# Kernel optimization log

Measured on AMD Instinct MI355X. Metric: run time of the kernel, lower is better.

## Reference

```python
import jax, jax.numpy as jnp
import numpy as np
from jax import lax


def squash(s):
    # scale = |s|^2/(1+|s|^2); out = scale * s/|s| (eps-stabilized as in source)
    norm = jnp.sum(s * s, axis=-1, keepdims=True)
    return (norm / (1.0 + norm)) * (s / jnp.sqrt(norm + 1e-8))


def setup_inputs() -> dict:
    key = jax.random.key(0)
    k = jax.random.split(key, 4)
    B, H, C = 32, 64, 10
    x = jax.random.normal(k[0], (B, 3, H, H), jnp.float32)
    conv1_w = jax.random.normal(k[1], (256, 3, 9, 9), jnp.float32) * 0.06
    conv1_b = jnp.zeros((256,), jnp.float32)
    conv2_w = jax.random.normal(k[2], (256, 256, 9, 9), jnp.float32) * 0.02  # 256 = 8 caps * 32 routes
    conv2_b = jnp.zeros((256,), jnp.float32)
    route_w = jax.random.normal(k[3], (32, C, 8, 16), jnp.float32)  # [routes, classes, in_dim, out_dim]
    return {"x": x, "conv1_w": conv1_w, "conv1_b": conv1_b,
            "conv2_w": conv2_w, "conv2_b": conv2_b, "route_w": route_w}


def reference(x, conv1_w, conv1_b, conv2_w, conv2_b, route_w):
    dn = ("NCHW", "OIHW", "NCHW")
    # PrimaryCapsules: conv 3->256 k9 s1 + relu
    h = lax.conv_general_dilated(x, conv1_w, (1, 1), "VALID", dimension_numbers=dn)
    h = jax.nn.relu(h + conv1_b[None, :, None, None])
    # CapsuleLayer conv: 256 -> 8*32 k9 s2
    h = lax.conv_general_dilated(h, conv2_w, (2, 2), "VALID", dimension_numbers=dn)
    h = h + conv2_b[None, :, None, None]
    B, _, hh, ww = h.shape
    R, D = 32, 8  # num_routes, capsule dim
    # [B, R*D, h, w] -> [B, R, P, D], squash per capsule vector
    caps = h.reshape(B, R, D, hh, ww).transpose(0, 1, 3, 4, 2).reshape(B, R, hh * ww, D)
    caps = squash(caps)
    # DigitCapsules: per-route linear maps 8->16, shared over spatial positions
    u_hat = jnp.einsum("brpi,rcio->brpco", caps, route_w)  # [B, R, P, C, 16]
    C, O = u_hat.shape[3], u_hat.shape[4]
    u_hat = u_hat.reshape(B, R * hh * ww, C, O)  # [B, N, C, 16]
    b_log = jnp.zeros(u_hat.shape[:-1], u_hat.dtype)  # [B, N, C]
    num_routing = 3
    v = None
    for i in range(num_routing):
        c = jax.nn.softmax(b_log, axis=2)            # over classes (dim=2 in source)
        s = jnp.einsum("bnc,bnco->bco", c, u_hat)    # weighted sum over input caps
        v = squash(s)                                 # [B, C, 16]
        if i < num_routing - 1:
            b_log = b_log + jnp.einsum("bnco,bco->bnc", u_hat, v)  # agreement
    return v
```

## Files before the change

kernel.cpp:

```cpp
#include <hip/hip_runtime.h>
#include <hip/hip_bf16.h>
#include <stdint.h>

typedef __attribute__((ext_vector_type(8))) short short8;
typedef __attribute__((ext_vector_type(4))) float f32x4;
typedef unsigned int u32x4a __attribute__((vector_size(16)));
typedef unsigned int u32x4u __attribute__((vector_size(16), aligned(4)));

__device__ inline unsigned short f2bf(float f) {
    union { float f; uint32_t u; } v; v.f = f;
    uint32_t u = v.u;
    uint32_t r = (u + 0x7FFFu + ((u >> 16) & 1u)) >> 16;
    return (unsigned short)r;
}

__device__ inline void gl_lds16(const unsigned short* g, unsigned short* l) {
    __builtin_amdgcn_global_load_lds(
        (const uint32_t __attribute__((address_space(1)))*)(const void*)g,
        (uint32_t __attribute__((address_space(3)))*)(void*)l, 16, 0, 0);
}

__global__ void cvt_w1(const float* __restrict__ w, unsigned short* __restrict__ A1) {
    int idx = blockIdx.x * 256 + threadIdx.x;
    int row = idx >> 8, k = idx & 255;
    float v = (k < 243) ? w[row * 243 + k] : 0.f;
    A1[idx] = f2bf(v);
}

__global__ void cvt_w2(const float* __restrict__ w, unsigned short* __restrict__ A2t) {
    int idx = blockIdx.x * 256 + threadIdx.x;
    int j = idx & 7;
    int off16 = (idx >> 3) & 1023;
    int tile = idx >> 13;
    int tm = tile / 324, chunk = tile - tm * 324;
    int row = off16 >> 3, sw = off16 & 7;
    int koct = sw ^ (row & 7);
    int kk = chunk * 64 + koct * 8 + j;
    int oc = tm * 128 + row;
    int ic, ky, kx;
    if (kk < 18432) { ic = kk / 72; int rem = kk - ic * 72; ky = rem >> 3; kx = rem & 7; }
    else { int j2 = kk - 18432; ic = j2 / 9; ky = j2 - ic * 9; kx = 8; }
    A2t[idx] = f2bf(w[((oc * 256 + ic) * 9 + ky) * 9 + kx]);
}

__global__ __launch_bounds__(256) void conv1_gemm(
    const unsigned short* __restrict__ A,
    const float* __restrict__ x,
    const float* __restrict__ bias,
    unsigned short* __restrict__ h1)
{
    __shared__ __align__(16) unsigned short As[128 * 40];
    __shared__ __align__(16) unsigned short Bs[128 * 40];
    const int tid = threadIdx.x;
    const int m0 = blockIdx.y * 128;
    const int n0 = blockIdx.x * 128;
    const int lane = tid & 63;
    const int wave = tid >> 6;
    const int wy = wave & 1, wx = wave >> 1;
    const int l16 = lane & 15, q = lane >> 4;

    const int kp = tid & 15;
    const int gn = tid >> 4;
    int baseN[8];
#pragma unroll
    for (int j = 0; j < 8; ++j) {
        int n = n0 + gn * 8 + j;
        int b = n / 3136, p = n % 3136;
        int oy = p / 56, ox = p % 56;
        baseN[j] = b * 12288 + oy * 64 + ox;
    }

    f32x4 acc[4][4];
#pragma unroll
    for (int im = 0; im < 4; ++im)
#pragma unroll
        for (int in = 0; in < 4; ++in)
            acc[im][in] = (f32x4){0.f, 0.f, 0.f, 0.f};

    for (int k0 = 0; k0 < 256; k0 += 32) {
        __syncthreads();
#pragma unroll
        for (int s = 0; s < 2; ++s) {
            int slot = tid + s * 256;
            int row = slot >> 2, seg = slot & 3;
            u32x4a v = *(const u32x4a*)(A + (m0 + row) * 256 + k0 + seg * 8);
            *(u32x4a*)(&As[row * 40 + seg * 8]) = v;
        }
        int ka = k0 + 2 * kp, kb = ka + 1;
        int offa = 0, offb = 0;
        bool va = ka < 243, vb = kb < 243;
        if (va) { int c = ka / 81, t = ka % 81, ky = t / 9, kx = t % 9; offa = c * 4096 + ky * 64 + kx; }
        if (vb) { int c = kb / 81, t = kb % 81, ky = t / 9, kx = t % 9; offb = c * 4096 + ky * 64 + kx; }
#pragma unroll
        for (int j = 0; j < 8; ++j) {
            unsigned int ba = va ? (unsigned int)f2bf(x[baseN[j] + offa]) : 0u;
            unsigned int bb = vb ? (unsigned int)f2bf(x[baseN[j] + offb]) : 0u;
            *(unsigned int*)(&Bs[(gn * 8 + j) * 40 + 2 * kp]) = ba | (bb << 16);
        }
        __syncthreads();

        short8 af[4], bf[4];
#pragma unroll
        for (int im = 0; im < 4; ++im)
            af[im] = *(const short8*)(&As[(wy * 64 + im * 16 + l16) * 40 + q * 8]);
#pragma unroll
        for (int in = 0; in < 4; ++in)
            bf[in] = *(const short8*)(&Bs[(wx * 64 + in * 16 + l16) * 40 + q * 8]);
#pragma unroll
        for (int im = 0; im < 4; ++im)
#pragma unroll
            for (int in = 0; in < 4; ++in)
                acc[im][in] = __builtin_amdgcn_mfma_f32_16x16x32_bf16(af[im], bf[in], acc[im][in], 0, 0, 0);
    }

#pragma unroll
    for (int in = 0; in < 4; ++in) {
        int n = n0 + wx * 64 + in * 16 + l16;
        int b = n / 3136, p = n % 3136;
        int oy = p / 56, ox = p % 56;
#pragma unroll
        for (int im = 0; im < 4; ++im) {
#pragma unroll
            for (int r = 0; r < 4; ++r) {
                int oc = m0 + wy * 64 + im * 16 + q * 4 + r;
                float v = acc[im][in][r] + bias[oc];
                v = v > 0.f ? v : 0.f;
                h1[((b * 256 + oc) * 56 + oy) * 56 + ox] = f2bf(v);
            }
        }
    }
}

__global__ __launch_bounds__(256) void conv2_gemm(
    const unsigned short* __restrict__ A2t,
    const unsigned short* __restrict__ h1,
    float* __restrict__ c2)
{
    __shared__ __align__(16) unsigned short As[2][8192];
    __shared__ __align__(16) unsigned short Bs[2][8192];
    const int tid = threadIdx.x;
    const int n0 = blockIdx.x * 128;
    const int z = blockIdx.z;
    const int lane = tid & 63;
    const int wave = tid >> 6;
    const int wy = wave & 1, wx = wave >> 1;
    const int l16 = lane & 15, q = lane >> 4;

    int bsrcA, bsrcB;
    {
        int ngA = n0 + lane;
        int bA = ngA / 576, pA = ngA % 576;
        bsrcA = bA * 802816 + (2 * (pA / 24)) * 56 + 2 * (pA % 24);
        int ngB = n0 + 64 + lane;
        int bB = ngB / 576, pB = ngB % 576;
        bsrcB = bB * 802816 + (2 * (pB / 24)) * 56 + 2 * (pB % 24);
    }
    const int tn = tid & 127, thalf = tid >> 7;
    int tbase;
    {
        int ng = n0 + tn;
        int b = ng / 576, p = ng % 576;
        tbase = b * 802816 + (2 * (p / 24)) * 56 + 2 * (p % 24) + 8;
    }

    f32x4 acc[4][4];
#pragma unroll
    for (int im = 0; im < 4; ++im)
#pragma unroll
        for (int in = 0; in < 4; ++in)
            acc[im][in] = (f32x4){0.f, 0.f, 0.f, 0.f};

    const size_t tilebase = (size_t)blockIdx.y * 324 * 8192;
    uint32_t bR[16];

    auto issueA = [&](int c, int buf) {
        const unsigned short* at = A2t + tilebase + (size_t)c * 8192;
        int s0 = wave * 4;
#pragma unroll
        for (int i = 0; i < 4; ++i) {
            int sl = (s0 + i) * 64 + lane;
            gl_lds16(at + sl * 8, &As[buf][sl * 8]);
        }
    };
    auto issueB = [&](int c, int buf) {
#pragma unroll
        for (int i = 0; i < 4; ++i) {
            int jp = wave * 4 + i;
            int octk = c * 8 + (jp >> 1);
            int ic = octk / 9, ky = octk - ic * 9;
            int src = ((jp & 1) ? bsrcB : bsrcA) + ic * 3136 + ky * 56;
            int sl = jp * 64 + lane;
            gl_lds16(h1 + src, &Bs[buf][sl * 8]);
        }
    };
    auto loadBtail = [&](int c) {
        int base = c * 64 + thalf * 32 - 18432;
#pragma unroll
        for (int p = 0; p < 16; ++p) {
            int j2 = base + 2 * p;
            int icA = j2 / 9, kyA = j2 - icA * 9;
            int icB = (j2 + 1) / 9, kyB = (j2 + 1) - icB * 9;
            uint32_t ba = h1[tbase + icA * 3136 + kyA * 56];
            uint32_t bb = h1[tbase + icB * 3136 + kyB * 56];
            bR[p] = ba | (bb << 16);
        }
    };
    auto writeBtail = [&](int buf) {
#pragma unroll
        for (int p = 0; p < 16; ++p) {
            int kk = thalf * 32 + 2 * p;
            int koct = kk >> 3, slot = kk & 7;
            *(uint32_t*)(&Bs[buf][(koct * 128 + tn) * 8 + slot]) = bR[p];
        }
    };

    const int nch = (324 - z + 7) >> 3;
    int c = z;
    issueA(c, 0);
    if (c < 288) issueB(c, 0); else loadBtail(c);
    for (int i = 0; i < nch; ++i) {
        const int cur = i & 1;
        const int cnext = c + 8;
        __syncthreads();
        if (c >= 288) { writeBtail(cur); __syncthreads(); }
        if (i + 1 < nch) {
            issueA(cnext, cur ^ 1);
            if (cnext < 288) issueB(cnext, cur ^ 1); else loadBtail(cnext);
        }
#pragma unroll
        for (int h = 0; h < 2; ++h) {
            short8 af[4], bf[4];
#pragma unroll
            for (int im = 0; im < 4; ++im) {
                int row = wy * 64 + im * 16 + l16;
                int koct = h * 4 + q;
                af[im] = *(const short8*)(&As[cur][(row * 8 + (koct ^ (row & 7))) * 8]);
            }
#pragma unroll
            for (int in = 0; in < 4; ++in)
                bf[in] = *(const short8*)(&Bs[cur][((h * 4 + q) * 128 + wx * 64 + in * 16 + l16) * 8]);
#pragma unroll
            for (int im = 0; im < 4; ++im)
#pragma unroll
                for (int in = 0; in < 4; ++in)
                    acc[im][in] = __builtin_amdgcn_mfma_f32_16x16x32_bf16(af[im], bf[in], acc[im][in], 0, 0, 0);
        }
        c = cnext;
    }

    const int m0 = blockIdx.y * 128;
#pragma unroll
    for (int in = 0; in < 4; ++in) {
        int nn = n0 + wx * 64 + in * 16 + l16;
        int bb = nn / 576, pp = nn % 576;
#pragma unroll
        for (int im = 0; im < 4; ++im) {
#pragma unroll
            for (int r = 0; r < 4; ++r) {
                int oc = m0 + wy * 64 + im * 16 + q * 4 + r;
                atomicAdd(&c2[(bb * 256 + oc) * 576 + pp], acc[im][in][r]);
            }
        }
    }
}

__global__ void squash_caps(const float* __restrict__ c2, const float* __restrict__ bias,
                            float* __restrict__ caps) {
    int idx = blockIdx.x * 256 + threadIdx.x;
    int b = idx / 18432;
    int rp = idx % 18432;
    int r = rp / 576, p = rp % 576;
    float s[8]; float n2 = 0.f;
#pragma unroll
    for (int d = 0; d < 8; ++d) {
        s[d] = c2[(b * 256 + r * 8 + d) * 576 + p] + bias[r * 8 + d];
        n2 += s[d] * s[d];
    }
    float sc = (n2 / (1.f + n2)) / sqrtf(n2 + 1e-8f);
#pragma unroll
    for (int d = 0; d < 8; ++d)
        caps[idx * 8 + d] = sc * s[d];
}

__global__ __launch_bounds__(64) void capsum0(const float* __restrict__ caps,
                                              float* __restrict__ G) {
    int r = blockIdx.x, b = blockIdx.y;
    const float* cp = caps + (size_t)(b * 32 + r) * 4608;
    int tid = threadIdx.x;
    f32x4 s0 = (f32x4){0.f, 0.f, 0.f, 0.f}, s1 = s0;
    for (int jv = 0; jv < 9; ++jv) {
        const f32x4* qp = (const f32x4*)(cp + (jv * 64 + tid) * 8);
        s0 += qp[0]; s1 += qp[1];
    }
#pragma unroll
    for (int off = 32; off > 0; off >>= 1) {
#pragma unroll
        for (int k = 0; k < 4; ++k) {
            s0[k] += __shfl_down(s0[k], off, 64);
            s1[k] += __shfl_down(s1[k], off, 64);
        }
    }
    if (tid == 0) {
        float g[8] = {s0[0], s0[1], s0[2], s0[3], s1[0], s1[1], s1[2], s1[3]};
        float* gp = G + (size_t)((b * 32 + r) * 10) * 8;
        for (int cc = 0; cc < 10; ++cc)
#pragma unroll
            for (int ii = 0; ii < 8; ++ii) gp[cc * 8 + ii] = g[ii] * 0.1f;
    }
}

__global__ __launch_bounds__(64) void route_accum(const float* __restrict__ caps,
                                                  const float* __restrict__ W,
                                                  const float* __restrict__ V,
                                                  float* __restrict__ G) {
    int r = blockIdx.x, b = blockIdx.y;
    __shared__ float wv[80];
    __shared__ float red[80][64];
    int tid = threadIdx.x;
    for (int v = tid; v < 80; v += 64) {
        int cc = v >> 3, ii = v & 7;
        float s = 0.f;
#pragma unroll
        for (int o = 0; o < 16; ++o)
            s += W[((r * 10 + cc) * 8 + ii) * 16 + o] * V[(b * 10 + cc) * 16 + o];
        wv[v] = s;
    }
    __syncthreads();
    float g[80];
#pragma unroll
    for (int v = 0; v < 80; ++v) g[v] = 0.f;
    const float* cp = caps + (size_t)(b * 32 + r) * 4608;
    for (int j = 0; j < 9; ++j) {
        int p = j * 64 + tid;
        const f32x4* qp = (const f32x4*)(cp + p * 8);
        f32x4 c0 = qp[0], c1 = qp[1];
        float c8[8];
#pragma unroll
        for (int i = 0; i < 4; ++i) { c8[i] = c0[i]; c8[4 + i] = c1[i]; }
        float a[10]; float m = -1e30f;
#pragma unroll
        for (int cc = 0; cc < 10; ++cc) {
            float t = 0.f;
#pragma unroll
            for (int i = 0; i < 8; ++i) t += c8[i] * wv[cc * 8 + i];
            a[cc] = t; m = fmaxf(m, t);
        }
        float sum = 0.f;
#pragma unroll
        for (int cc = 0; cc < 10; ++cc) { a[cc] = __expf(a[cc] - m); sum += a[cc]; }
        float inv = 1.f / sum;
#pragma unroll
        for (int cc = 0; cc < 10; ++cc) {
            float w = a[cc] * inv;
#pragma unroll
            for (int i = 0; i < 8; ++i) g[cc * 8 + i] += w * c8[i];
        }
    }
#pragma unroll
    for (int v = 0; v < 80; ++v) red[v][tid] = g[v];
    __syncthreads();
    for (int v = tid; v < 80; v += 64) {
        float s = 0.f;
        for (int t = 0; t < 64; ++t) s += red[v][t];
        G[(b * 32 + r) * 80 + v] = s;
    }
}

__global__ __launch_bounds__(160) void sv_kernel(const float* __restrict__ G,
                                                 const float* __restrict__ W,
                                                 float* __restrict__ V,
                                                 float* __restrict__ out, int last) {
    int b = blockIdx.x;
    int c = threadIdx.x / 16, o = threadIdx.x % 16;
    __shared__ float sL[10][16];
    float s = 0.f;
    for (int r = 0; r < 32; ++r) {
        const float* g = G + ((b * 32 + r) * 10 + c) * 8;
        const float* w = W + ((r * 10 + c) * 8) * 16 + o;
#pragma unroll
        for (int i = 0; i < 8; ++i) s += g[i] * w[i * 16];
    }
    sL[c][o] = s;
    __syncthreads();
    float n2 = 0.f;
#pragma unroll
    for (int oo = 0; oo < 16; ++oo) { float t = sL[c][oo]; n2 += t * t; }
    float sc = (n2 / (1.f + n2)) / sqrtf(n2 + 1e-8f);
    float v = sc * s;
    V[(b * 10 + c) * 16 + o] += v;
    if (last) out[(b * 10 + c) * 16 + o] = v;
}

extern "C" void kernel_launch(void* const* d_in, const int* in_sizes, int n_in,
                              void* d_out, int out_size, void* d_ws, size_t ws_size,
                              hipStream_t stream) {
    const float* x  = (const float*)d_in[0];
    const float* w1 = (const float*)d_in[1];
    const float* b1 = (const float*)d_in[2];
    const float* w2 = (const float*)d_in[3];
    const float* b2 = (const float*)d_in[4];
    const float* rw = (const float*)d_in[5];

    char* ws = (char*)d_ws;
    unsigned short* A1   = (unsigned short*)(ws);
    unsigned short* A2   = (unsigned short*)(ws + 262144);
    unsigned short* h1   = (unsigned short*)(ws + 10878976);
    float*          c2   = (float*)(ws + 62259200);
    float*          caps = (float*)(ws + 81133568);
    float*          V    = (float*)(ws + 100007936);
    float*          G    = (float*)(ws + 100028416);

    hipLaunchKernelGGL(cvt_w1, dim3(256), dim3(256), 0, stream, w1, A1);
    hipLaunchKernelGGL(cvt_w2, dim3(20736), dim3(256), 0, stream, w2, A2);
    hipMemsetAsync(c2, 0, 18874368, stream);
    hipLaunchKernelGGL(conv1_gemm, dim3(784, 2), dim3(256), 0, stream, A1, x, b1, h1);
    hipLaunchKernelGGL(conv2_gemm, dim3(144, 2, 8), dim3(256), 0, stream, A2, h1, c2);
    hipLaunchKernelGGL(squash_caps, dim3(2304), dim3(256), 0, stream, c2, b2, caps);
    hipMemsetAsync(V, 0, 5120 * sizeof(float), stream);
    hipLaunchKernelGGL(capsum0, dim3(32, 32), dim3(64), 0, stream, caps, G);
    hipLaunchKernelGGL(sv_kernel, dim3(32), dim3(160), 0, stream, G, rw, V, (float*)d_out, 0);
    for (int it = 1; it < 3; ++it) {
        hipLaunchKernelGGL(route_accum, dim3(32, 32), dim3(64), 0, stream, caps, rw, V, G);
        hipLaunchKernelGGL(sv_kernel, dim3(32), dim3(160), 0, stream, G, rw, V,
                           (float*)d_out, it == 2 ? 1 : 0);
    }
}
```

Measured before the change: 498.3 us.

## Split conv2 GEMM K-chunk into half-stage pipeline with smaller B buffer

The conv2 implicit-GEMM main loop is restructured so each K-chunk is processed in two halves. B is staged through a half-size buffer indexed by half, while A loads for the next chunk are split across the two halves. Shrinking LDS use, together with a launch-bounds hint for 3 blocks per SM, is meant to raise occupancy and overlap loads with MFMA work. The cost is an extra barrier per chunk and tighter register limits that could cause spills. The loop also hardcodes 36 main iterations, which holds only when z indexes the split-K slices as before.

```diff
diff --git a/kernel.cpp b/kernel.cpp
--- a/kernel.cpp
+++ b/kernel.cpp
@@ -131,13 +131,13 @@
     }
 }
 
-__global__ __launch_bounds__(256) void conv2_gemm(
+__global__ __launch_bounds__(256, 3) void conv2_gemm(
     const unsigned short* __restrict__ A2t,
     const unsigned short* __restrict__ h1,
     float* __restrict__ c2)
 {
     __shared__ __align__(16) unsigned short As[2][8192];
-    __shared__ __align__(16) unsigned short Bs[2][8192];
+    __shared__ __align__(16) unsigned short Bs[2][4096];
     const int tid = threadIdx.x;
     const int n0 = blockIdx.x * 128;
     const int z = blockIdx.z;
@@ -173,24 +173,23 @@
     const size_t tilebase = (size_t)blockIdx.y * 324 * 8192;
     uint32_t bR[16];
 
-    auto issueA = [&](int c, int buf) {
+    auto issueAh = [&](int c, int buf, int half) {
         const unsigned short* at = A2t + tilebase + (size_t)c * 8192;
-        int s0 = wave * 4;
-#pragma unroll
-        for (int i = 0; i < 4; ++i) {
-            int sl = (s0 + i) * 64 + lane;
+#pragma unroll
+        for (int i = 0; i < 2; ++i) {
+            int sl = (half * 8 + wave * 2 + i) * 64 + lane;
             gl_lds16(at + sl * 8, &As[buf][sl * 8]);
         }
     };
-    auto issueB = [&](int c, int buf) {
-#pragma unroll
-        for (int i = 0; i < 4; ++i) {
-            int jp = wave * 4 + i;
-            int octk = c * 8 + (jp >> 1);
+    auto issueB = [&](int c, int h) {
+#pragma unroll
+        for (int i = 0; i < 2; ++i) {
+            int j = wave * 2 + i;
+            int octl = j >> 1;
+            int octk = c * 8 + h * 4 + octl;
             int ic = octk / 9, ky = octk - ic * 9;
-            int src = ((jp & 1) ? bsrcB : bsrcA) + ic * 3136 + ky * 56;
-            int sl = jp * 64 + lane;
-            gl_lds16(h1 + src, &Bs[buf][sl * 8]);
+            int src = ((j & 1) ? bsrcB : bsrcA) + ic * 3136 + ky * 56;
+            gl_lds16(h1 + src, &Bs[h][(octl * 128 + (j & 1) * 64 + lane) * 8]);
         }
     };
     auto loadBtail = [&](int c) {
@@ -205,47 +204,63 @@
             bR[p] = ba | (bb << 16);
         }
     };
-    auto writeBtail = [&](int buf) {
+    auto writeBtail = [&]() {
 #pragma unroll
         for (int p = 0; p < 16; ++p) {
             int kk = thalf * 32 + 2 * p;
-            int koct = kk >> 3, slot = kk & 7;
-            *(uint32_t*)(&Bs[buf][(koct * 128 + tn) * 8 + slot]) = bR[p];
-        }
+            int koct = kk >> 3;
+            *(uint32_t*)(&Bs[koct >> 2][((koct & 3) * 128 + tn) * 8 + (kk & 7)]) = bR[p];
+        }
+    };
+    auto compute = [&](int h, int cur) {
+        short8 af[4], bf[4];
+        int koct = h * 4 + q;
+#pragma unroll
+        for (int im = 0; im < 4; ++im) {
+            int row = wy * 64 + im * 16 + l16;
+            af[im] = *(const short8*)(&As[cur][(row * 8 + (koct ^ (row & 7))) * 8]);
+        }
+#pragma unroll
+        for (int in = 0; in < 4; ++in)
+            bf[in] = *(const short8*)(&Bs[h][(q * 128 + wx * 64 + in * 16 + l16) * 8]);
+#pragma unroll
+        for (int im = 0; im < 4; ++im)
+#pragma unroll
+            for (int in = 0; in < 4; ++in)
+                acc[im][in] = __builtin_amdgcn_mfma_f32_16x16x32_bf16(af[im], bf[in], acc[im][in], 0, 0, 0);
     };
 
     const int nch = (324 - z + 7) >> 3;
     int c = z;
-    issueA(c, 0);
-    if (c < 288) issueB(c, 0); else loadBtail(c);
-    for (int i = 0; i < nch; ++i) {
-        const int cur = i & 1;
-        const int cnext = c + 8;
-        __syncthreads();
-        if (c >= 288) { writeBtail(cur); __syncthreads(); }
+    issueAh(c, 0, 0); issueAh(c, 0, 1);
+    issueB(c, 0);
+    for (int i = 0; i < 36; ++i) {
+        const int cur = i & 1, nxt = cur ^ 1;
+        const int cn = c + 8;
+        __syncthreads();
+        issueB(c, 1);
+        issueAh(cn, nxt, 0);
+        compute(0, cur);
+        __syncthreads();
+        if (i + 1 < 36) issueB(cn, 0);
+        else loadBtail(cn);
+        issueAh(cn, nxt, 1);
+        compute(1, cur);
+        c = cn;
+    }
+    for (int i = 36; i < nch; ++i) {
+        const int cur = i & 1, nxt = cur ^ 1;
+        const int cn = c + 8;
+        __syncthreads();
+        writeBtail();
+        __syncthreads();
         if (i + 1 < nch) {
-            issueA(cnext, cur ^ 1);
-            if (cnext < 288) issueB(cnext, cur ^ 1); else loadBtail(cnext);
-        }
-#pragma unroll
-        for (int h = 0; h < 2; ++h) {
-            short8 af[4], bf[4];
-#pragma unroll
-            for (int im = 0; im < 4; ++im) {
-                int row = wy * 64 + im * 16 + l16;
-                int koct = h * 4 + q;
-                af[im] = *(const short8*)(&As[cur][(row * 8 + (koct ^ (row & 7))) * 8]);
-            }
-#pragma unroll
-            for (int in = 0; in < 4; ++in)
-                bf[in] = *(const short8*)(&Bs[cur][((h * 4 + q) * 128 + wx * 64 + in * 16 + l16) * 8]);
-#pragma unroll
-            for (int im = 0; im < 4; ++im)
-#pragma unroll
-                for (int in = 0; in < 4; ++in)
-                    acc[im][in] = __builtin_amdgcn_mfma_f32_16x16x32_bf16(af[im], bf[in], acc[im][in], 0, 0, 0);
-        }
-        c = cnext;
+            issueAh(cn, nxt, 0); issueAh(cn, nxt, 1);
+            loadBtail(cn);
+        }
+        compute(0, cur);
+        compute(1, cur);
+        c = cn;
     }
 
     const int m0 = blockIdx.y * 128;
```

Result: faster. 470.9 us (-5.5%).

## Load conv2 A fragments directly from global in MFMA layout, drop A LDS

Applied to the files above, without the earlier changes.

Weight preprocessing now writes conv2's A operand in the exact per-lane MFMA fragment order. The GEMM then loads A fragments straight from global memory into registers instead of staging them through shared memory, which halves LDS usage. The main loop is split into a fixed 36-iteration phase for the regular B path and a tail phase, and launch bounds request 3 blocks per SM. This cuts LDS traffic and raises occupancy, at the cost of exposing global load latency for A inside each iteration and adding register pressure.

```diff
diff --git a/kernel.cpp b/kernel.cpp
--- a/kernel.cpp
+++ b/kernel.cpp
@@ -30,12 +30,15 @@
 __global__ void cvt_w2(const float* __restrict__ w, unsigned short* __restrict__ A2t) {
     int idx = blockIdx.x * 256 + threadIdx.x;
     int j = idx & 7;
-    int off16 = (idx >> 3) & 1023;
+    int l16 = (idx >> 3) & 15;
+    int q = (idx >> 7) & 3;
+    int h = (idx >> 9) & 1;
+    int im = (idx >> 10) & 3;
+    int wyh = (idx >> 12) & 1;
     int tile = idx >> 13;
     int tm = tile / 324, chunk = tile - tm * 324;
-    int row = off16 >> 3, sw = off16 & 7;
-    int koct = sw ^ (row & 7);
-    int kk = chunk * 64 + koct * 8 + j;
+    int row = wyh * 64 + im * 16 + l16;
+    int kk = chunk * 64 + (h * 4 + q) * 8 + j;
     int oc = tm * 128 + row;
     int ic, ky, kx;
     if (kk < 18432) { ic = kk / 72; int rem = kk - ic * 72; ky = rem >> 3; kx = rem & 7; }
@@ -131,12 +134,11 @@
     }
 }
 
-__global__ __launch_bounds__(256) void conv2_gemm(
+__global__ __launch_bounds__(256, 3) void conv2_gemm(
     const unsigned short* __restrict__ A2t,
     const unsigned short* __restrict__ h1,
     float* __restrict__ c2)
 {
-    __shared__ __align__(16) unsigned short As[2][8192];
     __shared__ __align__(16) unsigned short Bs[2][8192];
     const int tid = threadIdx.x;
     const int n0 = blockIdx.x * 128;
@@ -170,17 +172,17 @@
         for (int in = 0; in < 4; ++in)
             acc[im][in] = (f32x4){0.f, 0.f, 0.f, 0.f};
 
-    const size_t tilebase = (size_t)blockIdx.y * 324 * 8192;
+    const unsigned short* atile = A2t + (size_t)blockIdx.y * 324 * 8192 + wy * 4096 + lane * 8;
     uint32_t bR[16];
-
-    auto issueA = [&](int c, int buf) {
-        const unsigned short* at = A2t + tilebase + (size_t)c * 8192;
-        int s0 = wave * 4;
-#pragma unroll
-        for (int i = 0; i < 4; ++i) {
-            int sl = (s0 + i) * 64 + lane;
-            gl_lds16(at + sl * 8, &As[buf][sl * 8]);
-        }
+    short8 af[4][2];
+
+    auto loadA = [&](int c) {
+        const unsigned short* cb = atile + (size_t)c * 8192;
+#pragma unroll
+        for (int im = 0; im < 4; ++im)
+#pragma unroll
+            for (int h = 0; h < 2; ++h)
+                af[im][h] = *(const short8*)(cb + (im * 2 + h) * 512);
     };
     auto issueB = [&](int c, int buf) {
 #pragma unroll
@@ -189,8 +191,7 @@
             int octk = c * 8 + (jp >> 1);
             int ic = octk / 9, ky = octk - ic * 9;
             int src = ((jp & 1) ? bsrcB : bsrcA) + ic * 3136 + ky * 56;
-            int sl = jp * 64 + lane;
-            gl_lds16(h1 + src, &Bs[buf][sl * 8]);
+            gl_lds16(h1 + src, &Bs[buf][((jp >> 1) * 128 + (jp & 1) * 64 + lane) * 8]);
         }
     };
     auto loadBtail = [&](int c) {
@@ -209,43 +210,45 @@
 #pragma unroll
         for (int p = 0; p < 16; ++p) {
             int kk = thalf * 32 + 2 * p;
-            int koct = kk >> 3, slot = kk & 7;
-            *(uint32_t*)(&Bs[buf][(koct * 128 + tn) * 8 + slot]) = bR[p];
-        }
+            *(uint32_t*)(&Bs[buf][((kk >> 3) * 128 + tn) * 8 + (kk & 7)]) = bR[p];
+        }
+    };
+    auto compute = [&](int h, int buf) {
+        short8 bf[4];
+#pragma unroll
+        for (int in = 0; in < 4; ++in)
+            bf[in] = *(const short8*)(&Bs[buf][((h * 4 + q) * 128 + wx * 64 + in * 16 + l16) * 8]);
+#pragma unroll
+        for (int im = 0; im < 4; ++im)
+#pragma unroll
+            for (int in = 0; in < 4; ++in)
+                acc[im][in] = __builtin_amdgcn_mfma_f32_16x16x32_bf16(af[im][h], bf[in], acc[im][in], 0, 0, 0);
     };
 
     const int nch = (324 - z + 7) >> 3;
     int c = z;
-    issueA(c, 0);
-    if (c < 288) issueB(c, 0); else loadBtail(c);
-    for (int i = 0; i < nch; ++i) {
+    issueB(c, 0);
+    for (int i = 0; i < 36; ++i) {
+        const int cur = i & 1, nxt = cur ^ 1;
+        const int cn = c + 8;
+        __syncthreads();
+        loadA(c);
+        if (i + 1 < 36) issueB(cn, nxt);
+        else loadBtail(cn);
+        compute(0, cur);
+        compute(1, cur);
+        c = cn;
+    }
+    for (int i = 36; i < nch; ++i) {
         const int cur = i & 1;
-        const int cnext = c + 8;
         __syncthreads();
-        if (c >= 288) { writeBtail(cur); __syncthreads(); }
-        if (i + 1 < nch) {
-            issueA(cnext, cur ^ 1);
-            if (cnext < 288) issueB(cnext, cur ^ 1); else loadBtail(cnext);
-        }
-#pragma unroll
-        for (int h = 0; h < 2; ++h) {
-            short8 af[4], bf[4];
-#pragma unroll
-            for (int im = 0; im < 4; ++im) {
-                int row = wy * 64 + im * 16 + l16;
-                int koct = h * 4 + q;
-                af[im] = *(const short8*)(&As[cur][(row * 8 + (koct ^ (row & 7))) * 8]);
-            }
-#pragma unroll
-            for (int in = 0; in < 4; ++in)
-                bf[in] = *(const short8*)(&Bs[cur][((h * 4 + q) * 128 + wx * 64 + in * 16 + l16) * 8]);
-#pragma unroll
-            for (int im = 0; im < 4; ++im)
-#pragma unroll
-                for (int in = 0; in < 4; ++in)
-                    acc[im][in] = __builtin_amdgcn_mfma_f32_16x16x32_bf16(af[im], bf[in], acc[im][in], 0, 0, 0);
-        }
-        c = cnext;
+        writeBtail(cur);
+        __syncthreads();
+        loadA(c);
+        if (i + 1 < nch) loadBtail(c + 8);
+        compute(0, cur);
+        compute(1, cur);
+        c += 8;
     }
 
     const int m0 = blockIdx.y * 128;
```

After: 476.8 us. 1.05x faster.
